# Performance work log

Hardware: AMD Instinct MI355X
Metric: run time of the kernel (lower is better)

The kernel has to match this reference:

```python
import jax, jax.numpy as jnp
import numpy as np

# Fixed-point emulation: SharedFxpShift = 8 -> scale 256. Integer bit-shifts of the
# original int32/int8 pipeline are emulated in float32 (multiply/divide by 2^8) with
# int8 clamping, keeping the same dataflow (resblock -> pred head -> bin packing ->
# upsample -> (N,8,ch) child scatter) so a quantized kernel can be checked against it.
SHIFT = 256.0

def requant(x):
    # RequantFxpToScaledInt8: shift down and clamp to int8 range
    return jnp.clip(x * (1.0 / SHIFT), -128.0, 127.0)

def prelu(x, a):
    return jnp.where(x >= 0, x, a * x)

def resblock(x, w1, w2, a):
    # SparseResBlockIn32W8Out32: requant -> linear -> prelu -> requant -> linear -> +x
    h = requant(x)
    h = h @ w1.T
    h = prelu(h, a)
    h = requant(h)
    h = h @ w2.T
    return x + h

def setup_inputs() -> dict:
    key = jax.random.key(0)
    ks = jax.random.split(key, 16)
    N, CH = 50000, 256
    w = lambda k, shp: jax.random.normal(k, shp, dtype=jnp.float32) * 0.05
    return {
        'x': jax.random.normal(ks[0], (N, CH), dtype=jnp.float32) * SHIFT,
        'cur_bin': jax.random.randint(ks[1], (N, 8), 0, 2, dtype=jnp.int32),
        'w_dec1': w(ks[2], (CH, CH)),
        'w_dec2': w(ks[3], (CH, CH)),
        'a_dec': jax.random.uniform(ks[4], (1,), dtype=jnp.float32),
        'w_pconv': w(ks[5], (CH, CH)),
        'a_pconv': jax.random.uniform(ks[6], (1,), dtype=jnp.float32),
        'w_plin': w(ks[7], (255, CH)),
        'w_up1': w(ks[8], (CH, CH + 8)),
        'a_up1': jax.random.uniform(ks[9], (1,), dtype=jnp.float32),
        'w_ur1': w(ks[10], (CH, CH)),
        'w_ur2': w(ks[11], (CH, CH)),
        'a_ur': jax.random.uniform(ks[12], (1,), dtype=jnp.float32),
        'w_uout': w(ks[13], (2048, CH)),
    }

def reference(x, cur_bin, w_dec1, w_dec2, a_dec, w_pconv, a_pconv, w_plin,
              w_up1, a_up1, w_ur1, w_ur2, a_ur, w_uout):
    N, CH = x.shape
    binf = cur_bin.astype(jnp.float32)
    # dec: residual block
    rec = resblock(x, w_dec1, w_dec2, a_dec)
    # pred: requant -> conv+prelu -> requant -> linear(ch,255)
    h = requant(rec)
    h = prelu(h @ w_pconv.T, a_pconv)
    h = requant(h)
    cur_pred = h @ w_plin.T                                   # [N, 255]
    # bin -> octree symbol: (cur_bin << arange(8)).sum(1) - 1
    bin2oct = jnp.arange(8, dtype=jnp.int32)
    cur_oct = jnp.sum(cur_bin << bin2oct, axis=1).astype(jnp.int16) - 1  # [N]
    # upsample: cat(rec, bin << shift) -> requant -> lin+prelu -> resblock -> requant -> lin(ch*8)
    u = jnp.concatenate([rec, binf * SHIFT], axis=1)          # [N, CH+8]
    u = requant(u)
    u = prelu(u @ w_up1.T, a_up1)
    u = resblock(u, w_ur1, w_ur2, a_ur)
    u = requant(u)
    u = u @ w_uout.T                                          # [N, 8*CH]
    # child gather: original does reshape(N,8,CH)[cur_bin.bool()] (ragged);
    # we keep the dense [N,8,CH] with unoccupied children zeroed (jit-friendly).
    rec_out = u.reshape(N, 8, CH) * binf[:, :, None]
    return rec_out, cur_pred, cur_oct
```

## Files before the change

### kernel.cpp

```cpp
#include <hip/hip_runtime.h>

typedef __bf16 bf16x8 __attribute__((ext_vector_type(8)));
typedef float  f32x4  __attribute__((ext_vector_type(4)));

#define OFF_DEC1  0
#define OFF_DEC2  65536
#define OFF_PCONV 131072
#define OFF_PLIN  196608
#define OFF_UP1   262144
#define OFF_UR1   335872
#define OFF_UR2   401408
#define OFF_UOUT  466944
#define WB_TOTAL  991232

__device__ __align__(16) unsigned short g_wb[WB_TOTAL];

__device__ __forceinline__ unsigned short f2bf(float f) {
  union { float f; unsigned u; } c; c.f = f;
  unsigned u = c.u + 0x7FFFu + ((c.u >> 16) & 1u);
  return (unsigned short)(u >> 16);
}
__device__ __forceinline__ float bf2f(unsigned short b) {
  union { unsigned u; float f; } c; c.u = ((unsigned)b) << 16;
  return c.f;
}
__device__ __forceinline__ float reqf(float v) {
  return fminf(fmaxf(v * 0.00390625f, -128.f), 127.f);
}

__global__ void wconv_kernel(const float* __restrict__ wd1, const float* __restrict__ wd2,
                             const float* __restrict__ wpc, const float* __restrict__ wpl,
                             const float* __restrict__ wu1, const float* __restrict__ wr1,
                             const float* __restrict__ wr2, const float* __restrict__ wuo) {
  int t = blockIdx.x * 256 + threadIdx.x;
  if (t >= WB_TOTAL) return;
  const float* src; int local, Ksrc = 256, Msrc = 256, rowOff = 0;
  if      (t < OFF_DEC2)  { src = wd1; local = t; }
  else if (t < OFF_PCONV) { src = wd2; local = t - OFF_DEC2; }
  else if (t < OFF_PLIN)  { src = wpc; local = t - OFF_PCONV; }
  else if (t < OFF_UP1)   { src = wpl; local = t - OFF_PLIN; Msrc = 255; }
  else if (t < OFF_UR1)   { src = wu1; local = t - OFF_UP1; Ksrc = 264; }
  else if (t < OFF_UR2)   { src = wr1; local = t - OFF_UR1; }
  else if (t < OFF_UOUT)  { src = wr2; local = t - OFF_UR2; }
  else { local = t - OFF_UOUT; int c = local >> 16; local &= 65535; src = wuo; rowOff = c * 256; }
  const int s = local >> 13, j = local & 8191;
  const int kslot = j >> 11, m = (j >> 3) & 255, kk = j & 7;
  const int k = s * 32 + kslot * 8 + kk;
  float v = (m < Msrc && k < Ksrc) ? src[(size_t)(rowOff + m) * Ksrc + k] : 0.f;
  g_wb[t] = f2bf(v);
}


__device__ __forceinline__ void zero_acc(f32x4 (&acc)[4][4]) {
#pragma unroll
  for (int i = 0; i < 4; ++i)
#pragma unroll
    for (int j = 0; j < 4; ++j) acc[i][j] = (f32x4){0.f, 0.f, 0.f, 0.f};
}

__device__ __forceinline__ void prelu_acc(f32x4 (&acc)[4][4], float a) {
#pragma unroll
  for (int i = 0; i < 4; ++i)
#pragma unroll
    for (int j = 0; j < 4; ++j)
#pragma unroll
      for (int r = 0; r < 4; ++r) {
        float v = acc[i][j][r];
        acc[i][j][r] = v >= 0.f ? v : a * v;
      }
}

__device__ __forceinline__ void stageW(const unsigned short* __restrict__ src,
                                       unsigned short* dst, int tid) {
#pragma unroll
  for (int i = 0; i < 4; ++i)
    __builtin_amdgcn_global_load_lds(
        (const __attribute__((address_space(1))) unsigned*)(src + i * 2048 + tid * 8),
        (__attribute__((address_space(3))) unsigned*)(dst + i * 2048 + tid * 8),
        16, 0, 0);
}

__device__ __forceinline__ void mfma_slice(const unsigned short* wl, const unsigned short* sAct,
                                           int w, int l15, int lq, int kb, f32x4 (&acc)[4][4]) {
  bf16x8 af[4];
#pragma unroll
  for (int nt = 0; nt < 4; ++nt) {
    const int row = nt * 16 + l15;
    af[nt] = *(const bf16x8*)((const char*)sAct + row * 512 + (kb ^ ((row & 7) << 4)));
  }
#pragma unroll
  for (int mt = 0; mt < 4; ++mt) {
    bf16x8 bfr = *(const bf16x8*)(wl + lq * 2048 + (w * 64 + mt * 16 + l15) * 8);
#pragma unroll
    for (int nt = 0; nt < 4; ++nt)
      acc[mt][nt] = __builtin_amdgcn_mfma_f32_16x16x32_bf16(bfr, af[nt], acc[mt][nt], 0, 0, 0);
  }
}

template<int NKS, bool BIN_TAIL>
__device__ __forceinline__ void gemm_cnt(const unsigned short* __restrict__ wcur,
                                         const unsigned short* __restrict__ wnext,
                                         unsigned short*& wl, unsigned short*& wn,
                                         const unsigned short* sAct,
                                         const unsigned short* sBinA,
                                         int tid, int w, int l15, int lq,
                                         f32x4 (&acc)[4][4]) {
#pragma unroll
  for (int ks = 0; ks < NKS; ++ks) {
    if (ks < NKS - 1) {
      stageW(wcur + (ks + 1) * 8192, wn, tid);
      asm volatile("s_waitcnt vmcnt(4)" ::: "memory");
    } else if (wnext) {
      stageW(wnext, wn, tid);
      asm volatile("s_waitcnt vmcnt(4)" ::: "memory");
    } else {
      asm volatile("s_waitcnt vmcnt(0)" ::: "memory");
    }
    __builtin_amdgcn_sched_barrier(0);
    __builtin_amdgcn_s_setprio(1);
    if (BIN_TAIL && ks == NKS - 1) {
      bf16x8 af[4];
#pragma unroll
      for (int nt = 0; nt < 4; ++nt)
        af[nt] = *(const bf16x8*)(sBinA + (nt * 16 + l15) * 32 + lq * 8);
#pragma unroll
      for (int mt = 0; mt < 4; ++mt) {
        bf16x8 bfr = *(const bf16x8*)(wl + lq * 2048 + (w * 64 + mt * 16 + l15) * 8);
#pragma unroll
        for (int nt = 0; nt < 4; ++nt)
          acc[mt][nt] = __builtin_amdgcn_mfma_f32_16x16x32_bf16(bfr, af[nt], acc[mt][nt], 0, 0, 0);
      }
    } else {
      mfma_slice(wl, sAct, w, l15, lq, ks * 64 + lq * 16, acc);
    }
    __builtin_amdgcn_s_setprio(0);
    unsigned short* t2 = wl; wl = wn; wn = t2;
  }
}

__device__ __forceinline__ void stage_rq(const f32x4 (&acc)[4][4], unsigned short* dst,
                                         int w, int l15, int lq) {
#pragma unroll
  for (int nt = 0; nt < 4; ++nt) {
    const int row = nt * 16 + l15;
    const int swz = (row & 7) << 4;
#pragma unroll
    for (int mt = 0; mt < 4; ++mt) {
      const int ch2 = (w * 64 + mt * 16 + lq * 4) * 2;
      ushort4 b4;
      b4.x = f2bf(reqf(acc[mt][nt][0]));
      b4.y = f2bf(reqf(acc[mt][nt][1]));
      b4.z = f2bf(reqf(acc[mt][nt][2]));
      b4.w = f2bf(reqf(acc[mt][nt][3]));
      *(ushort4*)((char*)dst + row * 512 + (ch2 ^ swz)) = b4;
    }
  }
}

__global__ __launch_bounds__(256, 2) void fused_kernel(
    const float* __restrict__ x, const int* __restrict__ cur_bin,
    const float* __restrict__ a_dec, const float* __restrict__ a_pconv,
    const float* __restrict__ a_up1, const float* __restrict__ a_ur,
    float* __restrict__ out, int N)
{
  __shared__ __align__(16) unsigned short sA[64 * 256];
  __shared__ __align__(16) unsigned short sW0[8192];
  __shared__ __align__(16) unsigned short sW1[8192];
  __shared__ __align__(16) unsigned short sBinA[64 * 32];

  const int tid = threadIdx.x;
  const int w = tid >> 6, l = tid & 63;
  const int l15 = l & 15, lq = l >> 4;
  const int r0 = blockIdx.x * 64;
  const size_t PRED_BASE = (size_t)N * 2048;
  const size_t OCT_BASE  = PRED_BASE + (size_t)N * 255;

  const float A_DEC = a_dec[0], A_PCONV = a_pconv[0], A_UP1 = a_up1[0], A_UR = a_ur[0];

  unsigned short *wl = sW0, *wn = sW1;
  stageW(g_wb + OFF_DEC1, wl, tid);

  for (int i = tid; i < 64 * 32; i += 256) {
    const int row = i >> 5, j = i & 31;
    float bv = 0.f;
    if (j < 8 && (r0 + row) < N) bv = (float)cur_bin[(size_t)(r0 + row) * 8 + j];
    sBinA[i] = (j < 8) ? f2bf(bv) : (unsigned short)0;
  }
  if (tid < 64 && (r0 + tid) < N) {
    int s = 0;
#pragma unroll
    for (int j = 0; j < 8; ++j) s += cur_bin[(size_t)(r0 + tid) * 8 + j] << j;
    out[OCT_BASE + r0 + tid] = (float)(s - 1);
  }
#pragma unroll
  for (int it = 0; it < 16; ++it) {
    const int e = it * 1024 + tid * 4;
    const int row = e >> 8, col = e & 255;
    float4 xv = make_float4(0.f, 0.f, 0.f, 0.f);
    if ((r0 + row) < N) xv = *(const float4*)(x + (size_t)(r0 + row) * 256 + col);
    ushort4 b4;
    b4.x = f2bf(reqf(xv.x)); b4.y = f2bf(reqf(xv.y));
    b4.z = f2bf(reqf(xv.z)); b4.w = f2bf(reqf(xv.w));
    *(ushort4*)((char*)sA + row * 512 + ((col * 2) ^ ((row & 7) << 4))) = b4;
  }
  __syncthreads();

  f32x4 acc[4][4];

  zero_acc(acc);
  gemm_cnt<8, false>(g_wb + OFF_DEC1, g_wb + OFF_DEC2, wl, wn, sA, sBinA, tid, w, l15, lq, acc);
  prelu_acc(acc, A_DEC);
  __syncthreads();
  stage_rq(acc, sA, w, l15, lq);
  __syncthreads();

  zero_acc(acc);
  gemm_cnt<8, false>(g_wb + OFF_DEC2, g_wb + OFF_UP1, wl, wn, sA, sBinA, tid, w, l15, lq, acc);
  __syncthreads();
#pragma unroll
  for (int nt = 0; nt < 4; ++nt) {
    const int row = nt * 16 + l15;
    const int swz = (row & 7) << 4;
#pragma unroll
    for (int mt = 0; mt < 4; ++mt) {
      const int ch0 = w * 64 + mt * 16 + lq * 4;
      float4 xv = make_float4(0.f, 0.f, 0.f, 0.f);
      if ((r0 + row) < N) xv = *(const float4*)(x + (size_t)(r0 + row) * 256 + ch0);
      ushort4 b4;
      b4.x = f2bf(reqf(xv.x + acc[mt][nt][0]));
      b4.y = f2bf(reqf(xv.y + acc[mt][nt][1]));
      b4.z = f2bf(reqf(xv.z + acc[mt][nt][2]));
      b4.w = f2bf(reqf(xv.w + acc[mt][nt][3]));
      *(ushort4*)((char*)sA + row * 512 + ((ch0 * 2) ^ swz)) = b4;
    }
  }
  __syncthreads();

  unsigned u1p[4][4][2];
  zero_acc(acc);
  gemm_cnt<9, true>(g_wb + OFF_UP1, g_wb + OFF_PCONV, wl, wn, sA, sBinA, tid, w, l15, lq, acc);
  prelu_acc(acc, A_UP1);
#pragma unroll
  for (int i = 0; i < 4; ++i)
#pragma unroll
    for (int j = 0; j < 4; ++j)
#pragma unroll
      for (int p = 0; p < 2; ++p)
        u1p[i][j][p] = (unsigned)f2bf(acc[i][j][2 * p]) |
                       ((unsigned)f2bf(acc[i][j][2 * p + 1]) << 16);

  zero_acc(acc);
  gemm_cnt<8, false>(g_wb + OFF_PCONV, g_wb + OFF_PLIN, wl, wn, sA, sBinA, tid, w, l15, lq, acc);
  prelu_acc(acc, A_PCONV);
  __syncthreads();
  stage_rq(acc, sA, w, l15, lq);
  __syncthreads();

  zero_acc(acc);
  gemm_cnt<8, false>(g_wb + OFF_PLIN, g_wb + OFF_UR1, wl, wn, sA, sBinA, tid, w, l15, lq, acc);
#pragma unroll
  for (int nt = 0; nt < 4; ++nt) {
    const int row = nt * 16 + l15;
    if ((r0 + row) < N) {
      float* rp = out + PRED_BASE + (size_t)(r0 + row) * 255;
#pragma unroll
      for (int mt = 0; mt < 4; ++mt) {
        const int col0 = w * 64 + mt * 16 + lq * 4;
#pragma unroll
        for (int r = 0; r < 4; ++r)
          if (col0 + r < 255)
            rp[col0 + r] = acc[mt][nt][r];
      }
    }
  }
  __syncthreads();

#pragma unroll
  for (int nt = 0; nt < 4; ++nt) {
    const int row = nt * 16 + l15;
    const int swz = (row & 7) << 4;
#pragma unroll
    for (int mt = 0; mt < 4; ++mt) {
      const int ch2 = (w * 64 + mt * 16 + lq * 4) * 2;
      ushort4 b4;
      b4.x = f2bf(reqf(bf2f((unsigned short)(u1p[mt][nt][0]))));
      b4.y = f2bf(reqf(bf2f((unsigned short)(u1p[mt][nt][0] >> 16))));
      b4.z = f2bf(reqf(bf2f((unsigned short)(u1p[mt][nt][1]))));
      b4.w = f2bf(reqf(bf2f((unsigned short)(u1p[mt][nt][1] >> 16))));
      *(ushort4*)((char*)sA + row * 512 + (ch2 ^ swz)) = b4;
    }
  }
  __syncthreads();

  zero_acc(acc);
  gemm_cnt<8, false>(g_wb + OFF_UR1, g_wb + OFF_UR2, wl, wn, sA, sBinA, tid, w, l15, lq, acc);
  prelu_acc(acc, A_UR);
  __syncthreads();
  stage_rq(acc, sA, w, l15, lq);
  __syncthreads();

  zero_acc(acc);
  gemm_cnt<8, false>(g_wb + OFF_UR2, g_wb + OFF_UOUT, wl, wn, sA, sBinA, tid, w, l15, lq, acc);
#pragma unroll
  for (int i = 0; i < 4; ++i)
#pragma unroll
    for (int j = 0; j < 4; ++j) {
      acc[i][j][0] += bf2f((unsigned short)(u1p[i][j][0]));
      acc[i][j][1] += bf2f((unsigned short)(u1p[i][j][0] >> 16));
      acc[i][j][2] += bf2f((unsigned short)(u1p[i][j][1]));
      acc[i][j][3] += bf2f((unsigned short)(u1p[i][j][1] >> 16));
    }
  __syncthreads();
  stage_rq(acc, sA, w, l15, lq);
  __syncthreads();

#pragma unroll 1
  for (int c = 0; c < 8; ++c) {
    zero_acc(acc);
    const unsigned short* wnxt = (c < 7) ? (g_wb + OFF_UOUT + (c + 1) * 65536) : nullptr;
    gemm_cnt<8, false>(g_wb + OFF_UOUT + c * 65536, wnxt, wl, wn, sA, sBinA, tid, w, l15, lq, acc);
#pragma unroll
    for (int nt = 0; nt < 4; ++nt) {
      const int row = nt * 16 + l15;
      if ((r0 + row) < N) {
        const float m = sBinA[row * 32 + c] ? 1.f : 0.f;
        float* rp = out + (size_t)(r0 + row) * 2048 + c * 256;
#pragma unroll
        for (int mt = 0; mt < 4; ++mt) {
          const int ch0 = w * 64 + mt * 16 + lq * 4;
          f32x4 v;
          v[0] = acc[mt][nt][0] * m; v[1] = acc[mt][nt][1] * m;
          v[2] = acc[mt][nt][2] * m; v[3] = acc[mt][nt][3] * m;
          *(f32x4*)(rp + ch0) = v;
        }
      }
    }
  }
}

extern "C" void kernel_launch(void* const* d_in, const int* in_sizes, int n_in,
                              void* d_out, int out_size, void* d_ws, size_t ws_size,
                              hipStream_t stream) {
  const float* x        = (const float*)d_in[0];
  const int*   cur_bin  = (const int*)d_in[1];
  const float* w_dec1   = (const float*)d_in[2];
  const float* w_dec2   = (const float*)d_in[3];
  const float* a_dec    = (const float*)d_in[4];
  const float* w_pconv  = (const float*)d_in[5];
  const float* a_pconv  = (const float*)d_in[6];
  const float* w_plin   = (const float*)d_in[7];
  const float* w_up1    = (const float*)d_in[8];
  const float* a_up1    = (const float*)d_in[9];
  const float* w_ur1    = (const float*)d_in[10];
  const float* w_ur2    = (const float*)d_in[11];
  const float* a_ur     = (const float*)d_in[12];
  const float* w_uout   = (const float*)d_in[13];

  const int N = in_sizes[0] / 256;

  wconv_kernel<<<(WB_TOTAL + 255) / 256, 256, 0, stream>>>(
      w_dec1, w_dec2, w_pconv, w_plin, w_up1, w_ur1, w_ur2, w_uout);

  fused_kernel<<<(N + 63) / 64, 256, 0, stream>>>(
      x, cur_bin, a_dec, a_pconv, a_up1, a_ur, (float*)d_out, N);
}
```

Baseline: 263.7 us.

## Split output channels across eight waves with 512-thread blocks

Doubles the block to 512 threads so each of eight waves owns 32 output channels instead of 64, halving per-thread accumulators. The weight pre-pack layout is reordered so each wave stages and reads a contiguous 1024-element slice per k-step. This aims to raise occupancy and latency hiding, at the cost of more waves sharing each activation tile and more barrier participants. The same 64-row tile per block keeps the grid size unchanged.

```diff
diff --git a/kernel.cpp b/kernel.cpp
--- a/kernel.cpp
+++ b/kernel.cpp
@@ -44,23 +44,25 @@
   else if (t < OFF_UOUT)  { src = wr2; local = t - OFF_UR2; }
   else { local = t - OFF_UOUT; int c = local >> 16; local &= 65535; src = wuo; rowOff = c * 256; }
   const int s = local >> 13, j = local & 8191;
-  const int kslot = j >> 11, m = (j >> 3) & 255, kk = j & 7;
-  const int k = s * 32 + kslot * 8 + kk;
+  const int wv = j >> 10, lq = (j >> 8) & 3, mt = (j >> 7) & 1;
+  const int l15 = (j >> 3) & 15, kk = j & 7;
+  const int m = wv * 32 + mt * 16 + l15;
+  const int k = s * 32 + lq * 8 + kk;
   float v = (m < Msrc && k < Ksrc) ? src[(size_t)(rowOff + m) * Ksrc + k] : 0.f;
   g_wb[t] = f2bf(v);
 }
 
 
-__device__ __forceinline__ void zero_acc(f32x4 (&acc)[4][4]) {
-#pragma unroll
-  for (int i = 0; i < 4; ++i)
+__device__ __forceinline__ void zero_acc(f32x4 (&acc)[2][4]) {
+#pragma unroll
+  for (int i = 0; i < 2; ++i)
 #pragma unroll
     for (int j = 0; j < 4; ++j) acc[i][j] = (f32x4){0.f, 0.f, 0.f, 0.f};
 }
 
-__device__ __forceinline__ void prelu_acc(f32x4 (&acc)[4][4], float a) {
-#pragma unroll
-  for (int i = 0; i < 4; ++i)
+__device__ __forceinline__ void prelu_acc(f32x4 (&acc)[2][4], float a) {
+#pragma unroll
+  for (int i = 0; i < 2; ++i)
 #pragma unroll
     for (int j = 0; j < 4; ++j)
 #pragma unroll
@@ -71,17 +73,19 @@
 }
 
 __device__ __forceinline__ void stageW(const unsigned short* __restrict__ src,
-                                       unsigned short* dst, int tid) {
-#pragma unroll
-  for (int i = 0; i < 4; ++i)
+                                       unsigned short* dst, int w, int l) {
+#pragma unroll
+  for (int i = 0; i < 2; ++i) {
+    const int off = w * 1024 + i * 512 + l * 8;
     __builtin_amdgcn_global_load_lds(
-        (const __attribute__((address_space(1))) unsigned*)(src + i * 2048 + tid * 8),
-        (__attribute__((address_space(3))) unsigned*)(dst + i * 2048 + tid * 8),
+        (const __attribute__((address_space(1))) unsigned*)(src + off),
+        (__attribute__((address_space(3))) unsigned*)(dst + off),
         16, 0, 0);
+  }
 }
 
 __device__ __forceinline__ void mfma_slice(const unsigned short* wl, const unsigned short* sAct,
-                                           int w, int l15, int lq, int kb, f32x4 (&acc)[4][4]) {
+                                           int w, int l15, int lq, int kb, f32x4 (&acc)[2][4]) {
   bf16x8 af[4];
 #pragma unroll
   for (int nt = 0; nt < 4; ++nt) {
@@ -89,8 +93,8 @@
     af[nt] = *(const bf16x8*)((const char*)sAct + row * 512 + (kb ^ ((row & 7) << 4)));
   }
 #pragma unroll
-  for (int mt = 0; mt < 4; ++mt) {
-    bf16x8 bfr = *(const bf16x8*)(wl + lq * 2048 + (w * 64 + mt * 16 + l15) * 8);
+  for (int mt = 0; mt < 2; ++mt) {
+    bf16x8 bfr = *(const bf16x8*)(wl + w * 1024 + lq * 256 + mt * 128 + l15 * 8);
 #pragma unroll
     for (int nt = 0; nt < 4; ++nt)
       acc[mt][nt] = __builtin_amdgcn_mfma_f32_16x16x32_bf16(bfr, af[nt], acc[mt][nt], 0, 0, 0);
@@ -103,16 +107,16 @@
                                          unsigned short*& wl, unsigned short*& wn,
                                          const unsigned short* sAct,
                                          const unsigned short* sBinA,
-                                         int tid, int w, int l15, int lq,
-                                         f32x4 (&acc)[4][4]) {
+                                         int w, int l, int l15, int lq,
+                                         f32x4 (&acc)[2][4]) {
 #pragma unroll
   for (int ks = 0; ks < NKS; ++ks) {
     if (ks < NKS - 1) {
-      stageW(wcur + (ks + 1) * 8192, wn, tid);
-      asm volatile("s_waitcnt vmcnt(4)" ::: "memory");
+      stageW(wcur + (ks + 1) * 8192, wn, w, l);
+      asm volatile("s_waitcnt vmcnt(2)" ::: "memory");
     } else if (wnext) {
-      stageW(wnext, wn, tid);
-      asm volatile("s_waitcnt vmcnt(4)" ::: "memory");
+      stageW(wnext, wn, w, l);
+      asm volatile("s_waitcnt vmcnt(2)" ::: "memory");
     } else {
       asm volatile("s_waitcnt vmcnt(0)" ::: "memory");
     }
@@ -124,8 +128,8 @@
       for (int nt = 0; nt < 4; ++nt)
         af[nt] = *(const bf16x8*)(sBinA + (nt * 16 + l15) * 32 + lq * 8);
 #pragma unroll
-      for (int mt = 0; mt < 4; ++mt) {
-        bf16x8 bfr = *(const bf16x8*)(wl + lq * 2048 + (w * 64 + mt * 16 + l15) * 8);
+      for (int mt = 0; mt < 2; ++mt) {
+        bf16x8 bfr = *(const bf16x8*)(wl + w * 1024 + lq * 256 + mt * 128 + l15 * 8);
 #pragma unroll
         for (int nt = 0; nt < 4; ++nt)
           acc[mt][nt] = __builtin_amdgcn_mfma_f32_16x16x32_bf16(bfr, af[nt], acc[mt][nt], 0, 0, 0);
@@ -138,15 +142,15 @@
   }
 }
 
-__device__ __forceinline__ void stage_rq(const f32x4 (&acc)[4][4], unsigned short* dst,
+__device__ __forceinline__ void stage_rq(const f32x4 (&acc)[2][4], unsigned short* dst,
                                          int w, int l15, int lq) {
 #pragma unroll
   for (int nt = 0; nt < 4; ++nt) {
     const int row = nt * 16 + l15;
     const int swz = (row & 7) << 4;
 #pragma unroll
-    for (int mt = 0; mt < 4; ++mt) {
-      const int ch2 = (w * 64 + mt * 16 + lq * 4) * 2;
+    for (int mt = 0; mt < 2; ++mt) {
+      const int ch2 = (w * 32 + mt * 16 + lq * 4) * 2;
       ushort4 b4;
       b4.x = f2bf(reqf(acc[mt][nt][0]));
       b4.y = f2bf(reqf(acc[mt][nt][1]));
@@ -157,7 +161,7 @@
   }
 }
 
-__global__ __launch_bounds__(256, 2) void fused_kernel(
+__global__ __launch_bounds__(512, 4) void fused_kernel(
     const float* __restrict__ x, const int* __restrict__ cur_bin,
     const float* __restrict__ a_dec, const float* __restrict__ a_pconv,
     const float* __restrict__ a_up1, const float* __restrict__ a_ur,
@@ -178,9 +182,9 @@
   const float A_DEC = a_dec[0], A_PCONV = a_pconv[0], A_UP1 = a_up1[0], A_UR = a_ur[0];
 
   unsigned short *wl = sW0, *wn = sW1;
-  stageW(g_wb + OFF_DEC1, wl, tid);
-
-  for (int i = tid; i < 64 * 32; i += 256) {
+  stageW(g_wb + OFF_DEC1, wl, w, l);
+
+  for (int i = tid; i < 64 * 32; i += 512) {
     const int row = i >> 5, j = i & 31;
     float bv = 0.f;
     if (j < 8 && (r0 + row) < N) bv = (float)cur_bin[(size_t)(r0 + row) * 8 + j];
@@ -193,8 +197,8 @@
     out[OCT_BASE + r0 + tid] = (float)(s - 1);
   }
 #pragma unroll
-  for (int it = 0; it < 16; ++it) {
-    const int e = it * 1024 + tid * 4;
+  for (int it = 0; it < 8; ++it) {
+    const int e = it * 2048 + tid * 4;
     const int row = e >> 8, col = e & 255;
     float4 xv = make_float4(0.f, 0.f, 0.f, 0.f);
     if ((r0 + row) < N) xv = *(const float4*)(x + (size_t)(r0 + row) * 256 + col);
@@ -205,25 +209,25 @@
   }
   __syncthreads();
 
-  f32x4 acc[4][4];
-
-  zero_acc(acc);
-  gemm_cnt<8, false>(g_wb + OFF_DEC1, g_wb + OFF_DEC2, wl, wn, sA, sBinA, tid, w, l15, lq, acc);
+  f32x4 acc[2][4];
+
+  zero_acc(acc);
+  gemm_cnt<8, false>(g_wb + OFF_DEC1, g_wb + OFF_DEC2, wl, wn, sA, sBinA, w, l, l15, lq, acc);
   prelu_acc(acc, A_DEC);
   __syncthreads();
   stage_rq(acc, sA, w, l15, lq);
   __syncthreads();
 
   zero_acc(acc);
-  gemm_cnt<8, false>(g_wb + OFF_DEC2, g_wb + OFF_UP1, wl, wn, sA, sBinA, tid, w, l15, lq, acc);
+  gemm_cnt<8, false>(g_wb + OFF_DEC2, g_wb + OFF_UP1, wl, wn, sA, sBinA, w, l, l15, lq, acc);
   __syncthreads();
 #pragma unroll
   for (int nt = 0; nt < 4; ++nt) {
     const int row = nt * 16 + l15;
     const int swz = (row & 7) << 4;
 #pragma unroll
-    for (int mt = 0; mt < 4; ++mt) {
-      const int ch0 = w * 64 + mt * 16 + lq * 4;
+    for (int mt = 0; mt < 2; ++mt) {
+      const int ch0 = w * 32 + mt * 16 + lq * 4;
       float4 xv = make_float4(0.f, 0.f, 0.f, 0.f);
       if ((r0 + row) < N) xv = *(const float4*)(x + (size_t)(r0 + row) * 256 + ch0);
       ushort4 b4;
@@ -236,12 +240,12 @@
   }
   __syncthreads();
 
-  unsigned u1p[4][4][2];
-  zero_acc(acc);
-  gemm_cnt<9, true>(g_wb + OFF_UP1, g_wb + OFF_PCONV, wl, wn, sA, sBinA, tid, w, l15, lq, acc);
+  unsigned u1p[2][4][2];
+  zero_acc(acc);
+  gemm_cnt<9, true>(g_wb + OFF_UP1, g_wb + OFF_PCONV, wl, wn, sA, sBinA, w, l, l15, lq, acc);
   prelu_acc(acc, A_UP1);
 #pragma unroll
-  for (int i = 0; i < 4; ++i)
+  for (int i = 0; i < 2; ++i)
 #pragma unroll
     for (int j = 0; j < 4; ++j)
 #pragma unroll
@@ -250,22 +254,22 @@
                        ((unsigned)f2bf(acc[i][j][2 * p + 1]) << 16);
 
   zero_acc(acc);
-  gemm_cnt<8, false>(g_wb + OFF_PCONV, g_wb + OFF_PLIN, wl, wn, sA, sBinA, tid, w, l15, lq, acc);
+  gemm_cnt<8, false>(g_wb + OFF_PCONV, g_wb + OFF_PLIN, wl, wn, sA, sBinA, w, l, l15, lq, acc);
   prelu_acc(acc, A_PCONV);
   __syncthreads();
   stage_rq(acc, sA, w, l15, lq);
   __syncthreads();
 
   zero_acc(acc);
-  gemm_cnt<8, false>(g_wb + OFF_PLIN, g_wb + OFF_UR1, wl, wn, sA, sBinA, tid, w, l15, lq, acc);
+  gemm_cnt<8, false>(g_wb + OFF_PLIN, g_wb + OFF_UR1, wl, wn, sA, sBinA, w, l, l15, lq, acc);
 #pragma unroll
   for (int nt = 0; nt < 4; ++nt) {
     const int row = nt * 16 + l15;
     if ((r0 + row) < N) {
       float* rp = out + PRED_BASE + (size_t)(r0 + row) * 255;
 #pragma unroll
-      for (int mt = 0; mt < 4; ++mt) {
-        const int col0 = w * 64 + mt * 16 + lq * 4;
+      for (int mt = 0; mt < 2; ++mt) {
+        const int col0 = w * 32 + mt * 16 + lq * 4;
 #pragma unroll
         for (int r = 0; r < 4; ++r)
           if (col0 + r < 255)
@@ -280,8 +284,8 @@
     const int row = nt * 16 + l15;
     const int swz = (row & 7) << 4;
 #pragma unroll
-    for (int mt = 0; mt < 4; ++mt) {
-      const int ch2 = (w * 64 + mt * 16 + lq * 4) * 2;
+    for (int mt = 0; mt < 2; ++mt) {
+      const int ch2 = (w * 32 + mt * 16 + lq * 4) * 2;
       ushort4 b4;
       b4.x = f2bf(reqf(bf2f((unsigned short)(u1p[mt][nt][0]))));
       b4.y = f2bf(reqf(bf2f((unsigned short)(u1p[mt][nt][0] >> 16))));
@@ -293,16 +297,16 @@
   __syncthreads();
 
   zero_acc(acc);
-  gemm_cnt<8, false>(g_wb + OFF_UR1, g_wb + OFF_UR2, wl, wn, sA, sBinA, tid, w, l15, lq, acc);
+  gemm_cnt<8, false>(g_wb + OFF_UR1, g_wb + OFF_UR2, wl, wn, sA, sBinA, w, l, l15, lq, acc);
   prelu_acc(acc, A_UR);
   __syncthreads();
   stage_rq(acc, sA, w, l15, lq);
   __syncthreads();
 
   zero_acc(acc);
-  gemm_cnt<8, false>(g_wb + OFF_UR2, g_wb + OFF_UOUT, wl, wn, sA, sBinA, tid, w, l15, lq, acc);
-#pragma unroll
-  for (int i = 0; i < 4; ++i)
+  gemm_cnt<8, false>(g_wb + OFF_UR2, g_wb + OFF_UOUT, wl, wn, sA, sBinA, w, l, l15, lq, acc);
+#pragma unroll
+  for (int i = 0; i < 2; ++i)
 #pragma unroll
     for (int j = 0; j < 4; ++j) {
       acc[i][j][0] += bf2f((unsigned short)(u1p[i][j][0]));
@@ -318,7 +322,7 @@
   for (int c = 0; c < 8; ++c) {
     zero_acc(acc);
     const unsigned short* wnxt = (c < 7) ? (g_wb + OFF_UOUT + (c + 1) * 65536) : nullptr;
-    gemm_cnt<8, false>(g_wb + OFF_UOUT + c * 65536, wnxt, wl, wn, sA, sBinA, tid, w, l15, lq, acc);
+    gemm_cnt<8, false>(g_wb + OFF_UOUT + c * 65536, wnxt, wl, wn, sA, sBinA, w, l, l15, lq, acc);
 #pragma unroll
     for (int nt = 0; nt < 4; ++nt) {
       const int row = nt * 16 + l15;
@@ -326,8 +330,8 @@
         const float m = sBinA[row * 32 + c] ? 1.f : 0.f;
         float* rp = out + (size_t)(r0 + row) * 2048 + c * 256;
 #pragma unroll
-        for (int mt = 0; mt < 4; ++mt) {
-          const int ch0 = w * 64 + mt * 16 + lq * 4;
+        for (int mt = 0; mt < 2; ++mt) {
+          const int ch0 = w * 32 + mt * 16 + lq * 4;
           f32x4 v;
           v[0] = acc[mt][nt][0] * m; v[1] = acc[mt][nt][1] * m;
           v[2] = acc[mt][nt][2] * m; v[3] = acc[mt][nt][3] * m;
@@ -361,6 +365,6 @@
   wconv_kernel<<<(WB_TOTAL + 255) / 256, 256, 0, stream>>>(
       w_dec1, w_dec2, w_pconv, w_plin, w_up1, w_ur1, w_ur2, w_uout);
 
-  fused_kernel<<<(N + 63) / 64, 256, 0, stream>>>(
+  fused_kernel<<<(N + 63) / 64, 512, 0, stream>>>(
       x, cur_bin, a_dec, a_pconv, a_up1, a_ur, (float*)d_out, N);
 }
```

New measurement: 245.8 us. 6.8% less time.
